# Kernel optimization log

Measured on AMD Instinct MI355X. Metric: run time of the kernel, lower is better.

Reference implementation:

```python
import jax, jax.numpy as jnp
import numpy as np

N_HEAD = 8
HID = 64
IN_DIM = 512
OUT_DIM = 512


def setup_inputs() -> dict:
    key = jax.random.key(0)
    ks = jax.random.split(key, 12)
    B, LQ, LK = 2, 2048, 2048
    stdv = 1.0 / np.sqrt(HID)
    inp = {
        "q": jax.random.normal(ks[0], (B, LQ, IN_DIM), jnp.float32),
        "k": jax.random.normal(ks[1], (B, LK, IN_DIM), jnp.float32),
        "v": jax.random.normal(ks[2], (B, LK, IN_DIM), jnp.float32),
        # linear params stored as (in, out); torch Linear applies x @ W.T + b,
        # we store pre-transposed weights so y = x @ W + b is the same math.
        "Wq": jax.random.normal(ks[3], (IN_DIM, N_HEAD * HID), jnp.float32) * 0.02,
        "bq": jnp.zeros((N_HEAD * HID,), jnp.float32),
        "Wk": jax.random.normal(ks[4], (IN_DIM, N_HEAD * HID), jnp.float32) * 0.02,
        "bk": jnp.zeros((N_HEAD * HID,), jnp.float32),
        "Wv": jax.random.normal(ks[5], (IN_DIM, N_HEAD * HID), jnp.float32) * 0.02,
        "bv": jnp.zeros((N_HEAD * HID,), jnp.float32),
        # mlp-method scoring vector, uniform(-stdv, stdv), length 2*hidden
        "w_score": jax.random.uniform(ks[6], (2 * HID,), jnp.float32, -stdv, stdv),
        "Wd": jax.random.normal(ks[7], (N_HEAD * HID, OUT_DIM), jnp.float32) * 0.02,
        "bd": jnp.zeros((OUT_DIM,), jnp.float32),
    }
    return inp


def reference(q, k, v, Wq, bq, Wk, bk, Wv, bv, w_score, Wd, bd):
    B, Lq, _ = q.shape
    Lk = k.shape[1]
    # project and split heads -> (n_head, B, L, hid), matching torch's
    # permute(2,0,1,3).view(n_head*B, L, hid) layout
    qx = (q @ Wq + bq).reshape(B, Lq, N_HEAD, HID).transpose(2, 0, 1, 3)
    kx = (k @ Wk + bk).reshape(B, Lk, N_HEAD, HID).transpose(2, 0, 1, 3)
    vx = (v @ Wv + bv).reshape(B, Lk, N_HEAD, HID).transpose(2, 0, 1, 3)
    # 'mlp' additive attention: tanh(cat(q_i, k_j) . w) == tanh(q_i.w1 + k_j.w2)
    # computed as a broadcast sum instead of materializing the concat tensor
    w1, w2 = w_score[:HID], w_score[HID:]
    qw = qx @ w1  # (n_head, B, Lq)
    kw = kx @ w2  # (n_head, B, Lk)
    score = jnp.tanh(qw[..., :, None] + kw[..., None, :])  # (n_head, B, Lq, Lk)
    score = jax.nn.softmax(score, axis=-1)
    out_head = jnp.einsum('hbqk,hbkd->hbqd', score, vx)  # (n_head, B, Lq, hid)
    # torch: split along head*batch dim then cat along features -> head-major concat
    out = out_head.transpose(1, 2, 0, 3).reshape(B, Lq, N_HEAD * HID)
    output = out @ Wd + bd  # dropout is identity in eval
    score_flat = score.reshape(N_HEAD * B, Lq, Lk)
    return output, score_flat
```

## Files before the change

### kernel.cpp

```cpp
#include <hip/hip_runtime.h>
#include <math.h>

#define B_  2
#define L_  2048
#define D_  512
#define NH_ 8
#define HD_ 64

typedef __attribute__((ext_vector_type(8))) short short8;
typedef __attribute__((ext_vector_type(4))) float f32x4;

__device__ __forceinline__ float ex2(float x) {
#if __has_builtin(__builtin_amdgcn_exp2f)
    return __builtin_amdgcn_exp2f(x);
#else
    return exp2f(x);
#endif
}
__device__ __forceinline__ float rcp_(float x) {
#if __has_builtin(__builtin_amdgcn_rcpf)
    return __builtin_amdgcn_rcpf(x);
#else
    return 1.0f / x;
#endif
}

__device__ __forceinline__ float fast_e(float x) {
    float z  = ex2(x * 2.885390082f);
    float th = 1.0f - 2.0f * rcp_(z + 1.0f);
    return ex2(th * 1.4426950408889634f);
}

__device__ __forceinline__ unsigned int f2bf(float x) {
    unsigned int u = __float_as_uint(x);
    u += 0x7fffu + ((u >> 16) & 1u);
    return u >> 16;
}
__device__ __forceinline__ unsigned int pk2(float lo, float hi) {
    return f2bf(lo) | (f2bf(hi) << 16);
}

__global__ void k_prep(const float* __restrict__ Wq, const float* __restrict__ bq,
                       const float* __restrict__ Wk, const float* __restrict__ bk,
                       const float* __restrict__ wsc,
                       float* __restrict__ wqwT, float* __restrict__ wkwT,
                       float* __restrict__ bqw, float* __restrict__ bkw) {
    __shared__ float w[HD_];
    int which = blockIdx.x >> 1;
    int half  = blockIdx.x & 1;
    const float* W  = which ? Wk : Wq;
    const float* bb = which ? bk : bq;
    float* WT = which ? wkwT : wqwT;
    float* bo = which ? bkw  : bqw;
    if (threadIdx.x < HD_) w[threadIdx.x] = wsc[which * HD_ + threadIdx.x];
    __syncthreads();
    int r = half * 256 + threadIdx.x;
    for (int h = 0; h < NH_; ++h) {
        float s = 0.f;
        #pragma unroll 8
        for (int d = 0; d < HD_; ++d) s += W[r * D_ + h * HD_ + d] * w[d];
        WT[h * D_ + r] = s;
    }
    if (half == 0 && threadIdx.x < NH_) {
        int h = threadIdx.x;
        float s = 0.f;
        for (int d = 0; d < HD_; ++d) s += bb[h * HD_ + d] * w[d];
        bo[h] = s;
    }
}

__global__ void k_wconv(const float* __restrict__ Wv, const float* __restrict__ Wd,
                        unsigned short* __restrict__ WvF,
                        unsigned short* __restrict__ WdFh,
                        unsigned short* __restrict__ WdFl) {
    int id = blockIdx.x * 256 + threadIdx.x;
    int lane = id & 63;
    int kb = (id >> 6) & 15;
    int nf = id >> 10;
    int l15 = lane & 15, lg = lane >> 4;
    int n = nf * 16 + l15;
    int k0 = kb * 32 + lg * 4;
    size_t base = ((size_t)(nf * 16 + kb) * 64 + lane) * 8;
    if (blockIdx.y == 0) {
        #pragma unroll
        for (int j = 0; j < 8; ++j) {
            int k = k0 + (j & 3) + 16 * (j >> 2);
            WvF[base + j] = (unsigned short)f2bf(Wv[(size_t)k * 512 + n]);
        }
    } else {
        #pragma unroll
        for (int j = 0; j < 8; ++j) {
            int k = k0 + (j & 3) + 16 * (j >> 2);
            float x = Wd[(size_t)k * 512 + n];
            unsigned int h = f2bf(x);
            float hf = __uint_as_float(h << 16);
            WdFh[base + j] = (unsigned short)h;
            WdFl[base + j] = (unsigned short)f2bf(x - hf);
        }
    }
}

__global__ void k_qwkw(const float* __restrict__ q, const float* __restrict__ k,
                       const float* __restrict__ wqwT, const float* __restrict__ wkwT,
                       const float* __restrict__ bqw, const float* __restrict__ bkw,
                       float* __restrict__ qw, float* __restrict__ kw) {
    int wid  = blockIdx.x * 4 + (threadIdx.x >> 6);
    int lane = threadIdx.x & 63;
    int sel  = wid >= 4096;
    int row  = wid & 4095;
    const float* src = sel ? k : q;
    const float* WT  = sel ? wkwT : wqwT;
    const float* bo  = sel ? bkw : bqw;
    float* dst = sel ? kw : qw;
    float4 va = *(const float4*)(src + (size_t)row * D_ + lane * 4);
    float4 vb = *(const float4*)(src + (size_t)row * D_ + 256 + lane * 4);
    float res[NH_];
    #pragma unroll
    for (int h = 0; h < NH_; ++h) {
        float4 wa = *(const float4*)(WT + h * D_ + lane * 4);
        float4 wb = *(const float4*)(WT + h * D_ + 256 + lane * 4);
        float s = va.x*wa.x + va.y*wa.y + va.z*wa.z + va.w*wa.w
                + vb.x*wb.x + vb.y*wb.y + vb.z*wb.z + vb.w*wb.w;
        #pragma unroll
        for (int off = 32; off; off >>= 1) s += __shfl_xor(s, off);
        res[h] = s + bo[h];
    }
    if (lane == 0) {
        #pragma unroll
        for (int h = 0; h < NH_; ++h) dst[h * 4096 + row] = res[h];
    }
}

__global__ __launch_bounds__(256) void k_mmA(const float* __restrict__ A,
                                             const short8* __restrict__ BF,
                                             const float* __restrict__ bias,
                                             unsigned short* __restrict__ vxg) {
    int m0 = blockIdx.x * 128;
    int n0q = blockIdx.y * 4;
    int tid = threadIdx.x;
    int w = tid >> 6, lane = tid & 63;
    int l15 = lane & 15, lg = lane >> 4;
    f32x4 acc[2][4];
    #pragma unroll
    for (int i = 0; i < 2; ++i)
        #pragma unroll
        for (int j = 0; j < 4; ++j) acc[i][j] = (f32x4){0.f, 0.f, 0.f, 0.f};

    const float* a0 = A + (size_t)(m0 + w * 32 + l15) * 512 + lg * 4;
    const float* a1 = a0 + (size_t)16 * 512;

    for (int kb = 0; kb < 16; ++kb) {
        union { unsigned int u[4]; short8 s; } af0, af1;
        float4 lo0 = *(const float4*)(a0 + kb * 32);
        float4 hi0 = *(const float4*)(a0 + kb * 32 + 16);
        float4 lo1 = *(const float4*)(a1 + kb * 32);
        float4 hi1 = *(const float4*)(a1 + kb * 32 + 16);
        af0.u[0] = pk2(lo0.x, lo0.y); af0.u[1] = pk2(lo0.z, lo0.w);
        af0.u[2] = pk2(hi0.x, hi0.y); af0.u[3] = pk2(hi0.z, hi0.w);
        af1.u[0] = pk2(lo1.x, lo1.y); af1.u[1] = pk2(lo1.z, lo1.w);
        af1.u[2] = pk2(hi1.x, hi1.y); af1.u[3] = pk2(hi1.z, hi1.w);
        #pragma unroll
        for (int nf = 0; nf < 4; ++nf) {
            short8 bb = BF[((size_t)(n0q + nf) * 16 + kb) * 64 + lane];
            acc[0][nf] = __builtin_amdgcn_mfma_f32_16x16x32_bf16(af0.s, bb, acc[0][nf], 0, 0, 0);
            acc[1][nf] = __builtin_amdgcn_mfma_f32_16x16x32_bf16(af1.s, bb, acc[1][nf], 0, 0, 0);
        }
    }
    #pragma unroll
    for (int nf = 0; nf < 4; ++nf) {
        int n = (n0q + nf) * 16 + l15;
        float bvv = bias[n];
        int h = n >> 6, dt = (n >> 4) & 3, ncol = n & 15;
        #pragma unroll
        for (int mf = 0; mf < 2; ++mf) {
            #pragma unroll
            for (int r = 0; r < 4; ++r) {
                int m = m0 + w * 32 + mf * 16 + lg * 4 + r;
                int b = m >> 11, kk = m & 2047;
                int kblk = kk >> 5, k32 = kk & 31;
                int lane_v = ncol + 16 * ((k32 >> 2) & 3);
                int ie = (k32 & 3) + 4 * (k32 >> 4);
                size_t ad = ((((size_t)(h * 2 + b) * 64 + kblk) * 4 + dt) * 64 + lane_v) * 8 + ie;
                vxg[ad] = (unsigned short)f2bf(acc[mf][nf][r] + bvv);
            }
        }
    }
}

__global__ __launch_bounds__(256) void k_mmB(const float* __restrict__ A,
                                             const short8* __restrict__ BFh,
                                             const short8* __restrict__ BFl,
                                             const float* __restrict__ bias,
                                             float* __restrict__ C) {
    int m0 = blockIdx.x * 128;
    int n0q = blockIdx.y * 4;
    int tid = threadIdx.x;
    int w = tid >> 6, lane = tid & 63;
    int l15 = lane & 15, lg = lane >> 4;
    f32x4 acc[2][4];
    #pragma unroll
    for (int i = 0; i < 2; ++i)
        #pragma unroll
        for (int j = 0; j < 4; ++j) acc[i][j] = (f32x4){0.f, 0.f, 0.f, 0.f};

    const float* a0 = A + (size_t)(m0 + w * 32 + l15) * 512 + lg * 4;

    for (int kb = 0; kb < 16; ++kb) {
        union { unsigned int u[4]; short8 s; } ah[2], al[2];
        #pragma unroll
        for (int mf = 0; mf < 2; ++mf) {
            const float* ap = a0 + (size_t)mf * 16 * 512 + kb * 32;
            float4 lo = *(const float4*)ap;
            float4 hi = *(const float4*)(ap + 16);
            float xs[8] = {lo.x, lo.y, lo.z, lo.w, hi.x, hi.y, hi.z, hi.w};
            unsigned int hu[8]; float lf[8];
            #pragma unroll
            for (int j = 0; j < 8; ++j) {
                hu[j] = f2bf(xs[j]);
                lf[j] = xs[j] - __uint_as_float(hu[j] << 16);
            }
            #pragma unroll
            for (int j = 0; j < 4; ++j) {
                ah[mf].u[j] = hu[2 * j] | (hu[2 * j + 1] << 16);
                al[mf].u[j] = pk2(lf[2 * j], lf[2 * j + 1]);
            }
        }
        #pragma unroll
        for (int nf = 0; nf < 4; ++nf) {
            size_t bi = ((size_t)(n0q + nf) * 16 + kb) * 64 + lane;
            short8 bh = BFh[bi];
            short8 bl = BFl[bi];
            #pragma unroll
            for (int mf = 0; mf < 2; ++mf) {
                acc[mf][nf] = __builtin_amdgcn_mfma_f32_16x16x32_bf16(ah[mf].s, bh, acc[mf][nf], 0, 0, 0);
                acc[mf][nf] = __builtin_amdgcn_mfma_f32_16x16x32_bf16(al[mf].s, bh, acc[mf][nf], 0, 0, 0);
                acc[mf][nf] = __builtin_amdgcn_mfma_f32_16x16x32_bf16(ah[mf].s, bl, acc[mf][nf], 0, 0, 0);
            }
        }
    }
    #pragma unroll
    for (int nf = 0; nf < 4; ++nf) {
        int n = (n0q + nf) * 16 + l15;
        float bdv = bias[n];
        #pragma unroll
        for (int mf = 0; mf < 2; ++mf) {
            #pragma unroll
            for (int r = 0; r < 4; ++r) {
                int m = m0 + w * 32 + mf * 16 + lg * 4 + r;
                C[(size_t)m * 512 + n] = acc[mf][nf][r] + bdv;
            }
        }
    }
}

__global__ __launch_bounds__(256) void k_main(const float* __restrict__ qw,
                                              const float* __restrict__ kw,
                                              const short8* __restrict__ vgs,
                                              float* __restrict__ att,
                                              float* __restrict__ rsum_o) {
    int hb  = blockIdx.y;
    int q0  = blockIdx.x * 64;
    int tid = threadIdx.x;
    int wq  = tid >> 6;
    int lane = tid & 63;
    int l15 = lane & 15, lg = lane >> 4;

    __shared__ float kws[2048];
    *(float4*)&kws[tid * 8]     = *(const float4*)(kw + hb * 2048 + tid * 8);
    *(float4*)&kws[tid * 8 + 4] = *(const float4*)(kw + hb * 2048 + tid * 8 + 4);
    __syncthreads();

    float qwv = qw[hb * 2048 + q0 + wq * 16 + l15];
    const short8* bp = vgs + (size_t)hb * 16384 + lane;

    f32x4 acc0 = {0,0,0,0}, acc1 = {0,0,0,0}, acc2 = {0,0,0,0}, acc3 = {0,0,0,0};
    float sum = 0.f;

    for (int kblk = 0; kblk < 64; ++kblk) {
        int kidx = kblk * 32 + lg * 4;
        float4 kw0 = *(const float4*)&kws[kidx];
        float4 kw1 = *(const float4*)&kws[kidx + 16];
        float e0 = fast_e(qwv + kw0.x), e1 = fast_e(qwv + kw0.y);
        float e2 = fast_e(qwv + kw0.z), e3 = fast_e(qwv + kw0.w);
        float e4 = fast_e(qwv + kw1.x), e5 = fast_e(qwv + kw1.y);
        float e6 = fast_e(qwv + kw1.z), e7 = fast_e(qwv + kw1.w);
        sum += ((e0 + e1) + (e2 + e3)) + ((e4 + e5) + (e6 + e7));
        union { unsigned int u[4]; short8 s; } af;
        af.u[0] = pk2(e0, e1);
        af.u[1] = pk2(e2, e3);
        af.u[2] = pk2(e4, e5);
        af.u[3] = pk2(e6, e7);
        const short8* b = bp + kblk * 256;
        short8 b0 = b[0];
        short8 b1 = b[64];
        short8 b2 = b[128];
        short8 b3 = b[192];
        acc0 = __builtin_amdgcn_mfma_f32_16x16x32_bf16(af.s, b0, acc0, 0, 0, 0);
        acc1 = __builtin_amdgcn_mfma_f32_16x16x32_bf16(af.s, b1, acc1, 0, 0, 0);
        acc2 = __builtin_amdgcn_mfma_f32_16x16x32_bf16(af.s, b2, acc2, 0, 0, 0);
        acc3 = __builtin_amdgcn_mfma_f32_16x16x32_bf16(af.s, b3, acc3, 0, 0, 0);
    }

    sum += __shfl_xor(sum, 16);
    sum += __shfl_xor(sum, 32);
    float rs = 1.0f / sum;
    if (lane < 16) rsum_o[hb * 2048 + q0 + wq * 16 + lane] = rs;

    int b_ = hb & 1, h = hb >> 1;
    float r0s = __shfl(rs, lg * 4 + 0);
    float r1s = __shfl(rs, lg * 4 + 1);
    float r2s = __shfl(rs, lg * 4 + 2);
    float r3s = __shfl(rs, lg * 4 + 3);
    float* ab = att + ((size_t)(b_ * 2048 + q0 + wq * 16 + lg * 4)) * 512 + h * 64 + l15;
    #define ST_(dt, accv) \
        ab[0 * 512 + dt * 16] = accv[0] * r0s; \
        ab[1 * 512 + dt * 16] = accv[1] * r1s; \
        ab[2 * 512 + dt * 16] = accv[2] * r2s; \
        ab[3 * 512 + dt * 16] = accv[3] * r3s;
    ST_(0, acc0) ST_(1, acc1) ST_(2, acc2) ST_(3, acc3)
    #undef ST_
}

__global__ void k_score(const float* __restrict__ qw, const float* __restrict__ kw,
                        const float* __restrict__ rsum, float* __restrict__ score) {
    int hb = blockIdx.y;
    int tid = threadIdx.x;
    __shared__ float kws[2048];
    *(float4*)&kws[tid * 8]     = *(const float4*)(kw + hb * 2048 + tid * 8);
    *(float4*)&kws[tid * 8 + 4] = *(const float4*)(kw + hb * 2048 + tid * 8 + 4);
    __syncthreads();
    int rl  = tid >> 5;
    int t32 = tid & 31;
    int q = blockIdx.x * 8 + rl;
    float qwv = qw[hb * 2048 + q];
    float rs  = rsum[hb * 2048 + q];
    float* out = score + ((size_t)(hb * 2048 + q)) * 2048;
    #pragma unroll
    for (int i = 0; i < 16; ++i) {
        int k = i * 128 + t32 * 4;
        float4 o;
        o.x = fast_e(qwv + kws[k + 0]) * rs;
        o.y = fast_e(qwv + kws[k + 1]) * rs;
        o.z = fast_e(qwv + kws[k + 2]) * rs;
        o.w = fast_e(qwv + kws[k + 3]) * rs;
        *(float4*)(out + k) = o;
    }
}

extern "C" void kernel_launch(void* const* d_in, const int* in_sizes, int n_in,
                              void* d_out, int out_size, void* d_ws, size_t ws_size,
                              hipStream_t stream) {
    (void)in_sizes; (void)n_in; (void)out_size; (void)ws_size;
    const float* q   = (const float*)d_in[0];
    const float* k   = (const float*)d_in[1];
    const float* v   = (const float*)d_in[2];
    const float* Wq  = (const float*)d_in[3];
    const float* bq  = (const float*)d_in[4];
    const float* Wk  = (const float*)d_in[5];
    const float* bk  = (const float*)d_in[6];
    const float* Wv  = (const float*)d_in[7];
    const float* bv  = (const float*)d_in[8];
    const float* wsc = (const float*)d_in[9];
    const float* Wd  = (const float*)d_in[10];
    const float* bd  = (const float*)d_in[11];

    float* out   = (float*)d_out;
    float* score = out + (size_t)B_ * L_ * D_;

    float* ws    = (float*)d_ws;
    float* wqwT  = ws;
    float* wkwT  = ws + 4096;
    float* bqw   = ws + 8192;
    float* bkw   = ws + 8256;
    float* qw    = ws + 8704;
    float* kw    = ws + 41472;
    float* rsum  = ws + 74240;
    float* vxg   = ws + 107008;
    float* att   = ws + 1155584;
    float* WvF   = ws + 3252736;
    float* WdFh  = ws + 3383808;
    float* WdFl  = ws + 3514880;

    k_prep<<<dim3(4), dim3(256), 0, stream>>>(Wq, bq, Wk, bk, wsc, wqwT, wkwT, bqw, bkw);
    k_wconv<<<dim3(128, 2), dim3(256), 0, stream>>>(Wv, Wd,
        (unsigned short*)WvF, (unsigned short*)WdFh, (unsigned short*)WdFl);
    k_qwkw<<<dim3(2048), dim3(256), 0, stream>>>(q, k, wqwT, wkwT, bqw, bkw, qw, kw);
    k_mmA<<<dim3(32, 8), dim3(256), 0, stream>>>(v, (const short8*)WvF, bv,
        (unsigned short*)vxg);
    k_main<<<dim3(32, 16), dim3(256), 0, stream>>>(qw, kw, (const short8*)vxg, att, rsum);
    k_score<<<dim3(256, 16), dim3(256), 0, stream>>>(qw, kw, rsum, score);
    k_mmB<<<dim3(32, 8), dim3(256), 0, stream>>>(att, (const short8*)WdFh,
        (const short8*)WdFl, bd, out);
}
```

Baseline: 174.7 us.

## Split attention key range across wave pairs and shrink GEMM tiles with prefetch

k_main now runs 512 threads per block. Two wave groups each handle half of the key blocks, and their partial accumulators and row sums are combined through shared memory. The V-projection and output GEMMs use 64-row tiles, which doubles the grid, and they software-prefetch the next k-block's operands into registers. The intent is more parallelism and latency hiding on the dominant kernels, at the cost of an extra shared-memory reduction and barrier, and less operand reuse per wave in the GEMMs.

```diff
diff --git a/kernel.cpp b/kernel.cpp
--- a/kernel.cpp
+++ b/kernel.cpp
@@ -135,36 +135,40 @@
                                              const short8* __restrict__ BF,
                                              const float* __restrict__ bias,
                                              unsigned short* __restrict__ vxg) {
-    int m0 = blockIdx.x * 128;
+    int m0 = blockIdx.x * 64;
     int n0q = blockIdx.y * 4;
     int tid = threadIdx.x;
     int w = tid >> 6, lane = tid & 63;
     int l15 = lane & 15, lg = lane >> 4;
-    f32x4 acc[2][4];
-    #pragma unroll
-    for (int i = 0; i < 2; ++i)
-        #pragma unroll
-        for (int j = 0; j < 4; ++j) acc[i][j] = (f32x4){0.f, 0.f, 0.f, 0.f};
-
-    const float* a0 = A + (size_t)(m0 + w * 32 + l15) * 512 + lg * 4;
-    const float* a1 = a0 + (size_t)16 * 512;
+    f32x4 acc[4];
+    #pragma unroll
+    for (int j = 0; j < 4; ++j) acc[j] = (f32x4){0.f, 0.f, 0.f, 0.f};
+
+    const float* a0 = A + (size_t)(m0 + w * 16 + l15) * 512 + lg * 4;
+
+    float4 clo = *(const float4*)(a0);
+    float4 chi = *(const float4*)(a0 + 16);
+    short8 cb[4];
+    #pragma unroll
+    for (int nf = 0; nf < 4; ++nf) cb[nf] = BF[(size_t)(n0q + nf) * 16 * 64 + lane];
 
     for (int kb = 0; kb < 16; ++kb) {
-        union { unsigned int u[4]; short8 s; } af0, af1;
-        float4 lo0 = *(const float4*)(a0 + kb * 32);
-        float4 hi0 = *(const float4*)(a0 + kb * 32 + 16);
-        float4 lo1 = *(const float4*)(a1 + kb * 32);
-        float4 hi1 = *(const float4*)(a1 + kb * 32 + 16);
-        af0.u[0] = pk2(lo0.x, lo0.y); af0.u[1] = pk2(lo0.z, lo0.w);
-        af0.u[2] = pk2(hi0.x, hi0.y); af0.u[3] = pk2(hi0.z, hi0.w);
-        af1.u[0] = pk2(lo1.x, lo1.y); af1.u[1] = pk2(lo1.z, lo1.w);
-        af1.u[2] = pk2(hi1.x, hi1.y); af1.u[3] = pk2(hi1.z, hi1.w);
-        #pragma unroll
-        for (int nf = 0; nf < 4; ++nf) {
-            short8 bb = BF[((size_t)(n0q + nf) * 16 + kb) * 64 + lane];
-            acc[0][nf] = __builtin_amdgcn_mfma_f32_16x16x32_bf16(af0.s, bb, acc[0][nf], 0, 0, 0);
-            acc[1][nf] = __builtin_amdgcn_mfma_f32_16x16x32_bf16(af1.s, bb, acc[1][nf], 0, 0, 0);
-        }
+        float4 lo = clo, hi = chi;
+        short8 b0 = cb[0], b1 = cb[1], b2 = cb[2], b3 = cb[3];
+        if (kb < 15) {
+            clo = *(const float4*)(a0 + (kb + 1) * 32);
+            chi = *(const float4*)(a0 + (kb + 1) * 32 + 16);
+            #pragma unroll
+            for (int nf = 0; nf < 4; ++nf)
+                cb[nf] = BF[((size_t)(n0q + nf) * 16 + kb + 1) * 64 + lane];
+        }
+        union { unsigned int u[4]; short8 s; } af;
+        af.u[0] = pk2(lo.x, lo.y); af.u[1] = pk2(lo.z, lo.w);
+        af.u[2] = pk2(hi.x, hi.y); af.u[3] = pk2(hi.z, hi.w);
+        acc[0] = __builtin_amdgcn_mfma_f32_16x16x32_bf16(af.s, b0, acc[0], 0, 0, 0);
+        acc[1] = __builtin_amdgcn_mfma_f32_16x16x32_bf16(af.s, b1, acc[1], 0, 0, 0);
+        acc[2] = __builtin_amdgcn_mfma_f32_16x16x32_bf16(af.s, b2, acc[2], 0, 0, 0);
+        acc[3] = __builtin_amdgcn_mfma_f32_16x16x32_bf16(af.s, b3, acc[3], 0, 0, 0);
     }
     #pragma unroll
     for (int nf = 0; nf < 4; ++nf) {
@@ -172,17 +176,14 @@
         float bvv = bias[n];
         int h = n >> 6, dt = (n >> 4) & 3, ncol = n & 15;
         #pragma unroll
-        for (int mf = 0; mf < 2; ++mf) {
-            #pragma unroll
-            for (int r = 0; r < 4; ++r) {
-                int m = m0 + w * 32 + mf * 16 + lg * 4 + r;
-                int b = m >> 11, kk = m & 2047;
-                int kblk = kk >> 5, k32 = kk & 31;
-                int lane_v = ncol + 16 * ((k32 >> 2) & 3);
-                int ie = (k32 & 3) + 4 * (k32 >> 4);
-                size_t ad = ((((size_t)(h * 2 + b) * 64 + kblk) * 4 + dt) * 64 + lane_v) * 8 + ie;
-                vxg[ad] = (unsigned short)f2bf(acc[mf][nf][r] + bvv);
-            }
+        for (int r = 0; r < 4; ++r) {
+            int m = m0 + w * 16 + lg * 4 + r;
+            int b = m >> 11, kk = m & 2047;
+            int kblk = kk >> 5, k32 = kk & 31;
+            int lane_v = ncol + 16 * ((k32 >> 2) & 3);
+            int ie = (k32 & 3) + 4 * (k32 >> 4);
+            size_t ad = ((((size_t)(h * 2 + b) * 64 + kblk) * 4 + dt) * 64 + lane_v) * 8 + ie;
+            vxg[ad] = (unsigned short)f2bf(acc[nf][r] + bvv);
         }
     }
 }
@@ -192,26 +193,28 @@
                                              const short8* __restrict__ BFl,
                                              const float* __restrict__ bias,
                                              float* __restrict__ C) {
-    int m0 = blockIdx.x * 128;
+    int m0 = blockIdx.x * 64;
     int n0q = blockIdx.y * 4;
     int tid = threadIdx.x;
     int w = tid >> 6, lane = tid & 63;
     int l15 = lane & 15, lg = lane >> 4;
-    f32x4 acc[2][4];
-    #pragma unroll
-    for (int i = 0; i < 2; ++i)
-        #pragma unroll
-        for (int j = 0; j < 4; ++j) acc[i][j] = (f32x4){0.f, 0.f, 0.f, 0.f};
-
-    const float* a0 = A + (size_t)(m0 + w * 32 + l15) * 512 + lg * 4;
+    f32x4 acc[4];
+    #pragma unroll
+    for (int j = 0; j < 4; ++j) acc[j] = (f32x4){0.f, 0.f, 0.f, 0.f};
+
+    const float* a0 = A + (size_t)(m0 + w * 16 + l15) * 512 + lg * 4;
+
+    float4 clo = *(const float4*)(a0);
+    float4 chi = *(const float4*)(a0 + 16);
 
     for (int kb = 0; kb < 16; ++kb) {
-        union { unsigned int u[4]; short8 s; } ah[2], al[2];
-        #pragma unroll
-        for (int mf = 0; mf < 2; ++mf) {
-            const float* ap = a0 + (size_t)mf * 16 * 512 + kb * 32;
-            float4 lo = *(const float4*)ap;
-            float4 hi = *(const float4*)(ap + 16);
+        float4 lo = clo, hi = chi;
+        if (kb < 15) {
+            clo = *(const float4*)(a0 + (kb + 1) * 32);
+            chi = *(const float4*)(a0 + (kb + 1) * 32 + 16);
+        }
+        union { unsigned int u[4]; short8 s; } ah, al;
+        {
             float xs[8] = {lo.x, lo.y, lo.z, lo.w, hi.x, hi.y, hi.z, hi.w};
             unsigned int hu[8]; float lf[8];
             #pragma unroll
@@ -221,8 +224,8 @@
             }
             #pragma unroll
             for (int j = 0; j < 4; ++j) {
-                ah[mf].u[j] = hu[2 * j] | (hu[2 * j + 1] << 16);
-                al[mf].u[j] = pk2(lf[2 * j], lf[2 * j + 1]);
+                ah.u[j] = hu[2 * j] | (hu[2 * j + 1] << 16);
+                al.u[j] = pk2(lf[2 * j], lf[2 * j + 1]);
             }
         }
         #pragma unroll
@@ -230,12 +233,9 @@
             size_t bi = ((size_t)(n0q + nf) * 16 + kb) * 64 + lane;
             short8 bh = BFh[bi];
             short8 bl = BFl[bi];
-            #pragma unroll
-            for (int mf = 0; mf < 2; ++mf) {
-                acc[mf][nf] = __builtin_amdgcn_mfma_f32_16x16x32_bf16(ah[mf].s, bh, acc[mf][nf], 0, 0, 0);
-                acc[mf][nf] = __builtin_amdgcn_mfma_f32_16x16x32_bf16(al[mf].s, bh, acc[mf][nf], 0, 0, 0);
-                acc[mf][nf] = __builtin_amdgcn_mfma_f32_16x16x32_bf16(ah[mf].s, bl, acc[mf][nf], 0, 0, 0);
-            }
+            acc[nf] = __builtin_amdgcn_mfma_f32_16x16x32_bf16(ah.s, bh, acc[nf], 0, 0, 0);
+            acc[nf] = __builtin_amdgcn_mfma_f32_16x16x32_bf16(al.s, bh, acc[nf], 0, 0, 0);
+            acc[nf] = __builtin_amdgcn_mfma_f32_16x16x32_bf16(ah.s, bl, acc[nf], 0, 0, 0);
         }
     }
     #pragma unroll
@@ -243,31 +243,31 @@
         int n = (n0q + nf) * 16 + l15;
         float bdv = bias[n];
         #pragma unroll
-        for (int mf = 0; mf < 2; ++mf) {
-            #pragma unroll
-            for (int r = 0; r < 4; ++r) {
-                int m = m0 + w * 32 + mf * 16 + lg * 4 + r;
-                C[(size_t)m * 512 + n] = acc[mf][nf][r] + bdv;
-            }
-        }
-    }
-}
-
-__global__ __launch_bounds__(256) void k_main(const float* __restrict__ qw,
-                                              const float* __restrict__ kw,
-                                              const short8* __restrict__ vgs,
-                                              float* __restrict__ att,
-                                              float* __restrict__ rsum_o) {
+        for (int r = 0; r < 4; ++r) {
+            int m = m0 + w * 16 + lg * 4 + r;
+            C[(size_t)m * 512 + n] = acc[nf][r] + bdv;
+        }
+    }
+}
+
+__global__ __launch_bounds__(512, 4) void k_main(const float* __restrict__ qw,
+                                                 const float* __restrict__ kw,
+                                                 const short8* __restrict__ vgs,
+                                                 float* __restrict__ att,
+                                                 float* __restrict__ rsum_o) {
     int hb  = blockIdx.y;
     int q0  = blockIdx.x * 64;
     int tid = threadIdx.x;
-    int wq  = tid >> 6;
+    int w   = tid >> 6;
+    int wq  = w & 3;
+    int kh  = w >> 2;
     int lane = tid & 63;
     int l15 = lane & 15, lg = lane >> 4;
 
     __shared__ float kws[2048];
-    *(float4*)&kws[tid * 8]     = *(const float4*)(kw + hb * 2048 + tid * 8);
-    *(float4*)&kws[tid * 8 + 4] = *(const float4*)(kw + hb * 2048 + tid * 8 + 4);
+    __shared__ float red[4][16][68];
+
+    *(float4*)&kws[tid * 4] = *(const float4*)(kw + hb * 2048 + tid * 4);
     __syncthreads();
 
     float qwv = qw[hb * 2048 + q0 + wq * 16 + l15];
@@ -276,10 +276,22 @@
     f32x4 acc0 = {0,0,0,0}, acc1 = {0,0,0,0}, acc2 = {0,0,0,0}, acc3 = {0,0,0,0};
     float sum = 0.f;
 
-    for (int kblk = 0; kblk < 64; ++kblk) {
-        int kidx = kblk * 32 + lg * 4;
-        float4 kw0 = *(const float4*)&kws[kidx];
-        float4 kw1 = *(const float4*)&kws[kidx + 16];
+    int kb0 = kh * 32;
+    const short8* pb = bp + (size_t)kb0 * 256;
+    short8 cb0 = pb[0], cb1 = pb[64], cb2 = pb[128], cb3 = pb[192];
+    float4 ckw0 = *(const float4*)&kws[kb0 * 32 + lg * 4];
+    float4 ckw1 = *(const float4*)&kws[kb0 * 32 + lg * 4 + 16];
+
+    for (int i = 0; i < 32; ++i) {
+        short8 b0 = cb0, b1 = cb1, b2 = cb2, b3 = cb3;
+        float4 kw0 = ckw0, kw1 = ckw1;
+        if (i < 31) {
+            const short8* nb = bp + (size_t)(kb0 + i + 1) * 256;
+            cb0 = nb[0]; cb1 = nb[64]; cb2 = nb[128]; cb3 = nb[192];
+            int nk = (kb0 + i + 1) * 32 + lg * 4;
+            ckw0 = *(const float4*)&kws[nk];
+            ckw1 = *(const float4*)&kws[nk + 16];
+        }
         float e0 = fast_e(qwv + kw0.x), e1 = fast_e(qwv + kw0.y);
         float e2 = fast_e(qwv + kw0.z), e3 = fast_e(qwv + kw0.w);
         float e4 = fast_e(qwv + kw1.x), e5 = fast_e(qwv + kw1.y);
@@ -290,11 +302,6 @@
         af.u[1] = pk2(e2, e3);
         af.u[2] = pk2(e4, e5);
         af.u[3] = pk2(e6, e7);
-        const short8* b = bp + kblk * 256;
-        short8 b0 = b[0];
-        short8 b1 = b[64];
-        short8 b2 = b[128];
-        short8 b3 = b[192];
         acc0 = __builtin_amdgcn_mfma_f32_16x16x32_bf16(af.s, b0, acc0, 0, 0, 0);
         acc1 = __builtin_amdgcn_mfma_f32_16x16x32_bf16(af.s, b1, acc1, 0, 0, 0);
         acc2 = __builtin_amdgcn_mfma_f32_16x16x32_bf16(af.s, b2, acc2, 0, 0, 0);
@@ -303,22 +310,44 @@
 
     sum += __shfl_xor(sum, 16);
     sum += __shfl_xor(sum, 32);
-    float rs = 1.0f / sum;
-    if (lane < 16) rsum_o[hb * 2048 + q0 + wq * 16 + lane] = rs;
-
-    int b_ = hb & 1, h = hb >> 1;
-    float r0s = __shfl(rs, lg * 4 + 0);
-    float r1s = __shfl(rs, lg * 4 + 1);
-    float r2s = __shfl(rs, lg * 4 + 2);
-    float r3s = __shfl(rs, lg * 4 + 3);
-    float* ab = att + ((size_t)(b_ * 2048 + q0 + wq * 16 + lg * 4)) * 512 + h * 64 + l15;
-    #define ST_(dt, accv) \
-        ab[0 * 512 + dt * 16] = accv[0] * r0s; \
-        ab[1 * 512 + dt * 16] = accv[1] * r1s; \
-        ab[2 * 512 + dt * 16] = accv[2] * r2s; \
-        ab[3 * 512 + dt * 16] = accv[3] * r3s;
-    ST_(0, acc0) ST_(1, acc1) ST_(2, acc2) ST_(3, acc3)
-    #undef ST_
+
+    if (kh == 1) {
+        #define WR_(dt, accv) \
+            red[wq][lg * 4 + 0][dt * 16 + l15] = accv[0]; \
+            red[wq][lg * 4 + 1][dt * 16 + l15] = accv[1]; \
+            red[wq][lg * 4 + 2][dt * 16 + l15] = accv[2]; \
+            red[wq][lg * 4 + 3][dt * 16 + l15] = accv[3];
+        WR_(0, acc0) WR_(1, acc1) WR_(2, acc2) WR_(3, acc3)
+        #undef WR_
+        if (lane < 16) red[wq][lane][64] = sum;
+    }
+    __syncthreads();
+    if (kh == 0) {
+        #define RD_(dt, accv) \
+            accv[0] += red[wq][lg * 4 + 0][dt * 16 + l15]; \
+            accv[1] += red[wq][lg * 4 + 1][dt * 16 + l15]; \
+            accv[2] += red[wq][lg * 4 + 2][dt * 16 + l15]; \
+            accv[3] += red[wq][lg * 4 + 3][dt * 16 + l15];
+        RD_(0, acc0) RD_(1, acc1) RD_(2, acc2) RD_(3, acc3)
+        #undef RD_
+        float tot = sum + red[wq][l15][64];
+        float rs = 1.0f / tot;
+        if (lane < 16) rsum_o[hb * 2048 + q0 + wq * 16 + lane] = rs;
+
+        int b_ = hb & 1, h = hb >> 1;
+        float r0s = __shfl(rs, lg * 4 + 0);
+        float r1s = __shfl(rs, lg * 4 + 1);
+        float r2s = __shfl(rs, lg * 4 + 2);
+        float r3s = __shfl(rs, lg * 4 + 3);
+        float* ab = att + ((size_t)(b_ * 2048 + q0 + wq * 16 + lg * 4)) * 512 + h * 64 + l15;
+        #define ST_(dt, accv) \
+            ab[0 * 512 + dt * 16] = accv[0] * r0s; \
+            ab[1 * 512 + dt * 16] = accv[1] * r1s; \
+            ab[2 * 512 + dt * 16] = accv[2] * r2s; \
+            ab[3 * 512 + dt * 16] = accv[3] * r3s;
+        ST_(0, acc0) ST_(1, acc1) ST_(2, acc2) ST_(3, acc3)
+        #undef ST_
+    }
 }
 
 __global__ void k_score(const float* __restrict__ qw, const float* __restrict__ kw,
@@ -385,10 +414,10 @@
     k_wconv<<<dim3(128, 2), dim3(256), 0, stream>>>(Wv, Wd,
         (unsigned short*)WvF, (unsigned short*)WdFh, (unsigned short*)WdFl);
     k_qwkw<<<dim3(2048), dim3(256), 0, stream>>>(q, k, wqwT, wkwT, bqw, bkw, qw, kw);
-    k_mmA<<<dim3(32, 8), dim3(256), 0, stream>>>(v, (const short8*)WvF, bv,
+    k_mmA<<<dim3(64, 8), dim3(256), 0, stream>>>(v, (const short8*)WvF, bv,
         (unsigned short*)vxg);
-    k_main<<<dim3(32, 16), dim3(256), 0, stream>>>(qw, kw, (const short8*)vxg, att, rsum);
+    k_main<<<dim3(32, 16), dim3(512), 0, stream>>>(qw, kw, (const short8*)vxg, att, rsum);
     k_score<<<dim3(256, 16), dim3(256), 0, stream>>>(qw, kw, rsum, score);
-    k_mmB<<<dim3(32, 8), dim3(256), 0, stream>>>(att, (const short8*)WdFh,
+    k_mmB<<<dim3(64, 8), dim3(256), 0, stream>>>(att, (const short8*)WdFh,
         (const short8*)WdFl, bd, out);
 }
```

Result: faster. 164.1 us (-6.0%).
